# Optimization experiments

Hardware: AMD Instinct MI355X
Metric: run time of the kernel (lower is better)

The kernel has to match this reference:

```python
import jax, jax.numpy as jnp
import numpy as np

B, NORB, N_UP, N_DN, HIDDEN = 1024, 128, 32, 32, 4096


def setup_inputs() -> dict:
    rng = np.random.default_rng(0)
    # Build valid occupancy configs: exactly N_UP up-electrons (bit 0) and
    # N_DN down-electrons (bit 1) per sample. Encoding: 0=empty,1=up,2=dn,3=updn.
    up_order = np.argsort(rng.random((B, NORB)), axis=1)
    dn_order = np.argsort(rng.random((B, NORB)), axis=1)
    up_bit = np.zeros((B, NORB), np.int32)
    dn_bit = np.zeros((B, NORB), np.int32)
    np.put_along_axis(up_bit, up_order[:, :N_UP], 1, axis=1)
    np.put_along_axis(dn_bit, dn_order[:, :N_DN], 1, axis=1)
    x = jnp.asarray(up_bit + 2 * dn_bit, dtype=jnp.int32)

    key = jax.random.key(0)
    k1, k2, k3 = jax.random.split(key, 3)
    orbitals = jax.random.normal(k1, (NORB, N_UP), jnp.float32)
    W1 = jax.random.normal(k2, (4 * NORB, HIDDEN), jnp.float32) / np.sqrt(4 * NORB)
    b1 = jnp.zeros((HIDDEN,), jnp.float32)
    W2 = jax.random.normal(k3, (HIDDEN, NORB * N_UP), jnp.float32) / np.sqrt(HIDDEN)
    b2 = jnp.zeros((NORB * N_UP,), jnp.float32)
    return {"x": x, "orbitals": orbitals, "W1": W1, "b1": b1, "W2": W2, "b2": b2}


def _occupancies_to_electrons(x, n_up, n_dn):
    # Per-spin sorted positions of occupied orbitals. Stable argsort on the
    # inverted mask keeps occupied sites first, in ascending orbital order.
    up_mask = (x & 1) == 1
    dn_mask = (x & 2) == 2
    y_up = jnp.argsort(jnp.where(up_mask, 0, 1), axis=-1, stable=True)[:, :n_up]
    y_dn = jnp.argsort(jnp.where(dn_mask, 0, 1), axis=-1, stable=True)[:, :n_dn]
    return y_up, y_dn


def reference(x, orbitals, W1, b1, W2, b2):
    Bsz, norb = x.shape
    n_up = orbitals.shape[1]

    # correction_fun: MLP on one-hot config -> [B, norb, n_up]
    h = jax.nn.one_hot(x, 4, dtype=W1.dtype).reshape(Bsz, -1)  # [B, 4*norb]
    h = jax.nn.relu(h @ W1 + b1)                               # [B, hidden]
    corrections = (h @ W2 + b2).reshape(Bsz, norb, n_up)       # [B, norb, n_up]

    y_up, y_dn = _occupancies_to_electrons(x, n_up, n_up)
    y_up = y_up[..., None]  # [B, n_up, 1]
    y_dn = y_dn[..., None]

    # gather orbital rows + correction rows per electron (spin-symmetric orbitals)
    phi_up = jnp.take_along_axis(orbitals[None], y_up, axis=1)  # [B, n_up, n_up]
    phi_dn = jnp.take_along_axis(orbitals[None], y_dn, axis=1)
    d_up = jnp.take_along_axis(corrections, y_up, axis=1)
    d_dn = jnp.take_along_axis(corrections, y_dn, axis=1)

    s_up, log_det_up = jnp.linalg.slogdet(phi_up + d_up)
    s_dn, log_det_dn = jnp.linalg.slogdet(phi_dn + d_dn)
    return log_det_up + log_det_dn + jnp.log(s_up * s_dn + 0j)  # complex [B]
```

## Files before the change

### kernel.cpp

```cpp
#include <hip/hip_runtime.h>
#include <cmath>

#define B_SZ  1024
#define NORB  128
#define NUP   32
#define HID   4096
#define NCORR (NORB * NUP)
#define K1    (4 * NORB)

typedef short  bf16x8 __attribute__((ext_vector_type(8)));
typedef float  f32x4  __attribute__((ext_vector_type(4)));

__device__ __forceinline__ unsigned short f2bf_rne(float f) {
    unsigned int u = __float_as_uint(f);
    u += 0x7FFFu + ((u >> 16) & 1u);
    return (unsigned short)(u >> 16);
}

__global__ __launch_bounds__(256) void k_packx(const int* __restrict__ x,
                                               unsigned int* __restrict__ xp) {
    int t = threadIdx.x;
    int row = blockIdx.x * 32 + (t >> 3);
    int d = t & 7;
    const int* src = x + row * NORB + d * 16;
    unsigned int dw = 0;
#pragma unroll
    for (int b = 0; b < 16; ++b) dw |= ((unsigned int)(src[b] & 3)) << (2 * b);
    xp[row * 8 + d] = dw;
}

__global__ __launch_bounds__(256) void k_splitW(const float* __restrict__ W,
                                                unsigned short* __restrict__ Bph,
                                                unsigned short* __restrict__ Bpl,
                                                int ktTot) {
    __shared__ float tile[64][33];
    int n0 = blockIdx.x * 32, k0 = blockIdx.y * 64;
    int t = threadIdx.x;
    int nl = t & 31, kg = t >> 5;
#pragma unroll
    for (int i = 0; i < 8; ++i) {
        int kl = kg + i * 8;
        tile[kl][nl] = W[(size_t)(k0 + kl) * 4096 + n0 + nl];
    }
    __syncthreads();

    int nt = (n0 + nl) >> 4;
    int kt = (k0 >> 5) + (kg >> 2);
    int lane_o = (kg & 3) * 16 + (nl & 15);
    size_t o = (((size_t)nt * ktTot + kt) * 64 + lane_o) * 8;

    unsigned short hi8[8], lo8[8];
#pragma unroll
    for (int j = 0; j < 8; ++j) {
        float v = tile[kg * 8 + j][nl];
        unsigned short hi = f2bf_rne(v);
        float fhi = __uint_as_float((unsigned int)hi << 16);
        hi8[j] = hi;
        lo8[j] = f2bf_rne(v - fhi);
    }
    *(bf16x8*)(Bph + o) = *(bf16x8*)hi8;
    *(bf16x8*)(Bpl + o) = *(bf16x8*)lo8;
}

__global__ __launch_bounds__(256) void k_hidden2(const unsigned int* __restrict__ xp,
                                                 const unsigned short* __restrict__ Bph,
                                                 const unsigned short* __restrict__ Bpl,
                                                 const float* __restrict__ b1,
                                                 unsigned short* __restrict__ h_hi,
                                                 unsigned short* __restrict__ h_lo) {
    __shared__ unsigned int sxp[64][8];

    int n0 = blockIdx.x * 128;
    int m0 = blockIdx.y * 64;
    int t = threadIdx.x;
    int w = t >> 6, lane = t & 63;
    int lm = lane & 15, kq = lane >> 4;
    int wn = w * 32;

#pragma unroll
    for (int i = 0; i < 2; ++i) {
        int idx = t + 256 * i;
        sxp[idx >> 3][idx & 7] = xp[(m0 + (idx >> 3)) * 8 + (idx & 7)];
    }
    __syncthreads();

    size_t nt0 = (size_t)((n0 + wn) >> 4);
    const unsigned short* bph = Bph + nt0 * (16 * 512) + (size_t)lane * 8;
    const unsigned short* bpl = Bpl + nt0 * (16 * 512) + (size_t)lane * 8;

    f32x4 acc[4][2] = {};

    bf16x8 nbh0 = *(const bf16x8*)(bph);
    bf16x8 nbh1 = *(const bf16x8*)(bph + 16 * 512);
    bf16x8 nbl0 = *(const bf16x8*)(bpl);
    bf16x8 nbl1 = *(const bf16x8*)(bpl + 16 * 512);

    for (int kt = 0; kt < 16; ++kt) {
        bf16x8 bh0 = nbh0, bh1 = nbh1, bl0 = nbl0, bl1 = nbl1;
        if (kt + 1 < 16) {
            nbh0 = *(const bf16x8*)(bph + (kt + 1) * 512);
            nbh1 = *(const bf16x8*)(bph + 16 * 512 + (kt + 1) * 512);
            nbl0 = *(const bf16x8*)(bpl + (kt + 1) * 512);
            nbl1 = *(const bf16x8*)(bpl + 16 * 512 + (kt + 1) * 512);
        }

        int i0 = kt * 8 + kq * 2;
        int dwIdx = i0 >> 4;
        int sh = (i0 & 15) * 2;
        bf16x8 af[4];
#pragma unroll
        for (int fm = 0; fm < 4; ++fm) {
            unsigned int dw = sxp[fm * 16 + lm][dwIdx];
            unsigned int c01 = (dw >> sh) & 0xFu;
            union { bf16x8 v; unsigned long long u[2]; } a;
            a.u[0] = 0x3F80ULL << ((c01 & 3u) * 16);
            a.u[1] = 0x3F80ULL << ((c01 >> 2) * 16);
            af[fm] = a.v;
        }

#pragma unroll
        for (int fm = 0; fm < 4; ++fm) {
            acc[fm][0] = __builtin_amdgcn_mfma_f32_16x16x32_bf16(af[fm], bh0, acc[fm][0], 0, 0, 0);
            acc[fm][0] = __builtin_amdgcn_mfma_f32_16x16x32_bf16(af[fm], bl0, acc[fm][0], 0, 0, 0);
            acc[fm][1] = __builtin_amdgcn_mfma_f32_16x16x32_bf16(af[fm], bh1, acc[fm][1], 0, 0, 0);
            acc[fm][1] = __builtin_amdgcn_mfma_f32_16x16x32_bf16(af[fm], bl1, acc[fm][1], 0, 0, 0);
        }
    }

#pragma unroll
    for (int fm = 0; fm < 4; ++fm)
#pragma unroll
        for (int fn = 0; fn < 2; ++fn) {
            int n = n0 + wn + fn * 16 + lm;
            float bv = b1[n];
#pragma unroll
            for (int r = 0; r < 4; ++r) {
                int m = m0 + fm * 16 + kq * 4 + r;
                float v = fmaxf(acc[fm][fn][r] + bv, 0.f);
                unsigned short hi = f2bf_rne(v);
                float fhi = __uint_as_float((unsigned int)hi << 16);
                h_hi[(size_t)m * HID + n] = hi;
                h_lo[(size_t)m * HID + n] = f2bf_rne(v - fhi);
            }
        }
}

__global__ __launch_bounds__(256) void k_hidden_f32(const int* __restrict__ x,
                                                    const float* __restrict__ W1,
                                                    const float* __restrict__ b1,
                                                    float* __restrict__ h) {
    int b = blockIdx.x, tid = threadIdx.x;
    __shared__ int sx[NORB];
    if (tid < NORB) sx[tid] = x[b * NORB + tid];
    __syncthreads();
    float acc[16];
#pragma unroll
    for (int u = 0; u < 16; ++u) acc[u] = b1[tid + 256 * u];
    for (int i = 0; i < NORB; ++i) {
        const float* row = W1 + (size_t)(4 * i + sx[i]) * HID;
#pragma unroll
        for (int u = 0; u < 16; ++u) acc[u] += row[tid + 256 * u];
    }
    float* hb = h + (size_t)b * HID;
#pragma unroll
    for (int u = 0; u < 16; ++u) hb[tid + 256 * u] = fmaxf(acc[u], 0.f);
}

#define GBM 64
#define GBN 128
#define LPAD 40

__global__ __launch_bounds__(256, 3) void k_gemm3(const unsigned short* __restrict__ Ah_g,
                                                  const unsigned short* __restrict__ Al_g,
                                                  const unsigned short* __restrict__ Bh_g,
                                                  const unsigned short* __restrict__ Bl_g,
                                                  const float* __restrict__ bias,
                                                  float* __restrict__ C) {
    __shared__ unsigned short Ah[GBM][LPAD], Al[GBM][LPAD];

    int n0 = blockIdx.x * GBN;
    int m0 = blockIdx.y * GBM;
    int t = threadIdx.x;
    int w = t >> 6, lane = t & 63;
    int lm = lane & 15, kq = lane >> 4;
    int wn = w * 32;

    int ma = t >> 2, ga = t & 3;
    const unsigned short* agh = Ah_g + (size_t)(m0 + ma) * HID + ga * 8;
    const unsigned short* agl = Al_g + (size_t)(m0 + ma) * HID + ga * 8;

    size_t nt0 = (size_t)((n0 + wn) >> 4);
    const unsigned short* bph = Bh_g + nt0 * 65536 + (size_t)lane * 8;
    const unsigned short* bpl = Bl_g + nt0 * 65536 + (size_t)lane * 8;

    f32x4 acc[4][2] = {};

    float4 vah = *(const float4*)(agh);
    float4 val = *(const float4*)(agl);

    for (int kt = 0; kt < 128; ++kt) {
        if (kt) __syncthreads();

        bf16x8 cbh0 = *(const bf16x8*)(bph + (size_t)kt * 512);
        bf16x8 cbh1 = *(const bf16x8*)(bph + 65536u + (size_t)kt * 512);
        bf16x8 cbl0 = *(const bf16x8*)(bpl + (size_t)kt * 512);
        bf16x8 cbl1 = *(const bf16x8*)(bpl + 65536u + (size_t)kt * 512);

        *(float4*)&Ah[ma][ga * 8] = vah;
        *(float4*)&Al[ma][ga * 8] = val;
        __syncthreads();

        if (kt + 1 < 128) {
            vah = *(const float4*)(agh + (kt + 1) * 32);
            val = *(const float4*)(agl + (kt + 1) * 32);
        }

        bf16x8 afh[4], afl[4];
#pragma unroll
        for (int fm = 0; fm < 4; ++fm) {
            afh[fm] = *(const bf16x8*)&Ah[fm * 16 + lm][kq * 8];
            afl[fm] = *(const bf16x8*)&Al[fm * 16 + lm][kq * 8];
        }

#pragma unroll
        for (int fm = 0; fm < 4; ++fm) {
            acc[fm][0] = __builtin_amdgcn_mfma_f32_16x16x32_bf16(afh[fm], cbh0, acc[fm][0], 0, 0, 0);
            acc[fm][0] = __builtin_amdgcn_mfma_f32_16x16x32_bf16(afl[fm], cbh0, acc[fm][0], 0, 0, 0);
            acc[fm][0] = __builtin_amdgcn_mfma_f32_16x16x32_bf16(afh[fm], cbl0, acc[fm][0], 0, 0, 0);
            acc[fm][1] = __builtin_amdgcn_mfma_f32_16x16x32_bf16(afh[fm], cbh1, acc[fm][1], 0, 0, 0);
            acc[fm][1] = __builtin_amdgcn_mfma_f32_16x16x32_bf16(afl[fm], cbh1, acc[fm][1], 0, 0, 0);
            acc[fm][1] = __builtin_amdgcn_mfma_f32_16x16x32_bf16(afh[fm], cbl1, acc[fm][1], 0, 0, 0);
        }
    }

#pragma unroll
    for (int fm = 0; fm < 4; ++fm)
#pragma unroll
        for (int fn = 0; fn < 2; ++fn) {
            int n = n0 + wn + fn * 16 + lm;
            float bv = bias[n];
#pragma unroll
            for (int r = 0; r < 4; ++r) {
                int m = m0 + fm * 16 + kq * 4 + r;
                C[(size_t)m * NCORR + n] = acc[fm][fn][r] + bv;
            }
        }
}

#define BM 64
#define BN 64
#define BK 32
__global__ __launch_bounds__(256) void k_gemm(const float* __restrict__ A,
                                              const float* __restrict__ Bm,
                                              const float* __restrict__ bias,
                                              float* __restrict__ C) {
    __shared__ float As[BK][68];
    __shared__ float Bs[BK][BN];
    int n0 = blockIdx.x * BN, m0 = blockIdx.y * BM;
    int tid = threadIdx.x;
    int tm = tid >> 4, tn = tid & 15;
    int am = tid >> 3, ak = (tid & 7) * 4;
    int bk = tid >> 4, bn = (tid & 15) * 4;
    float acc[4][4] = {};
    for (int k0 = 0; k0 < HID; k0 += BK) {
#pragma unroll
        for (int s = 0; s < 2; ++s) {
            int m = am + 32 * s;
            float4 v = *(const float4*)(A + (size_t)(m0 + m) * HID + k0 + ak);
            As[ak + 0][m] = v.x; As[ak + 1][m] = v.y;
            As[ak + 2][m] = v.z; As[ak + 3][m] = v.w;
        }
#pragma unroll
        for (int s = 0; s < 2; ++s) {
            int k = bk + 16 * s;
            float4 v = *(const float4*)(Bm + (size_t)(k0 + k) * NCORR + n0 + bn);
            *(float4*)&Bs[k][bn] = v;
        }
        __syncthreads();
#pragma unroll
        for (int kk = 0; kk < BK; ++kk) {
            float4 a = *(const float4*)&As[kk][tm * 4];
            float4 bv = *(const float4*)&Bs[kk][tn * 4];
            float av[4] = {a.x, a.y, a.z, a.w};
            float bb[4] = {bv.x, bv.y, bv.z, bv.w};
#pragma unroll
            for (int i = 0; i < 4; ++i)
#pragma unroll
                for (int j = 0; j < 4; ++j) acc[i][j] += av[i] * bb[j];
        }
        __syncthreads();
    }
#pragma unroll
    for (int i = 0; i < 4; ++i) {
        int m = m0 + tm * 4 + i;
        float4 o;
        o.x = acc[i][0] + bias[n0 + tn * 4 + 0];
        o.y = acc[i][1] + bias[n0 + tn * 4 + 1];
        o.z = acc[i][2] + bias[n0 + tn * 4 + 2];
        o.w = acc[i][3] + bias[n0 + tn * 4 + 3];
        *(float4*)(C + (size_t)m * NCORR + n0 + tn * 4) = o;
    }
}

__global__ __launch_bounds__(128) void k_det(const int* __restrict__ x,
                                             const float* __restrict__ orbitals,
                                             const float* __restrict__ corr,
                                             float* __restrict__ out,
                                             int imag_off) {
    int b = blockIdx.x, tid = threadIdx.x;
    __shared__ int sx[NORB];
    __shared__ int yup[NUP], ydn[NUP];
    __shared__ float M[2][NUP][NUP + 1];
    __shared__ float rlog[2];
    __shared__ int rneg[2];

    sx[tid] = x[b * NORB + tid];
    __syncthreads();

    int occ = sx[tid];
    if (occ & 1) {
        int r = 0;
        for (int i = 0; i < tid; ++i) r += sx[i] & 1;
        yup[r] = tid;
    }
    if (occ & 2) {
        int r = 0;
        for (int i = 0; i < tid; ++i) r += (sx[i] >> 1) & 1;
        ydn[r] = tid;
    }
    __syncthreads();

    const float* cb = corr + (size_t)b * NCORR;
    for (int idx = tid; idx < 2 * NUP * NUP; idx += 128) {
        int s = idx >> 10;
        int i = (idx >> 5) & 31;
        int j = idx & 31;
        int r = s ? ydn[i] : yup[i];
        M[s][i][j] = orbitals[r * NUP + j] + cb[r * NUP + j];
    }
    __syncthreads();

    int wv = tid >> 6, lane = tid & 63;
    float (*Mm)[NUP + 1] = M[wv];
    float logdet = 0.f;
    int neg = 0;

    for (int k = 0; k < NUP; ++k) {
        float v = (lane >= k && lane < NUP) ? fabsf(Mm[lane][k]) : -1.f;
        int pi = lane;
#pragma unroll
        for (int off = 32; off > 0; off >>= 1) {
            float v2 = __shfl_down(v, off);
            int p2 = __shfl_down(pi, off);
            if (v2 > v) { v = v2; pi = p2; }
        }
        int p = __shfl(pi, 0);

        if (p != k) {
            if (lane < NUP) {
                float t1 = Mm[k][lane];
                Mm[k][lane] = Mm[p][lane];
                Mm[p][lane] = t1;
            }
            neg ^= 1;
        }
        __syncthreads();

        float pv = Mm[k][k];
        logdet += logf(fabsf(pv));
        if (pv < 0.f) neg ^= 1;

        int row = k + 1 + (lane & 31);
        int half = lane >> 5;
        if (row < NUP) {
            float f = Mm[row][k] / pv;
            for (int j = k + 1 + half; j < NUP; j += 2)
                Mm[row][j] -= f * Mm[k][j];
        }
        __syncthreads();
    }

    if (lane == 0) { rlog[wv] = logdet; rneg[wv] = neg; }
    __syncthreads();
    if (tid == 0) {
        out[b] = rlog[0] + rlog[1];
        if (imag_off > 0)
            out[imag_off + b] =
                (rneg[0] ^ rneg[1]) ? 3.14159265358979323846f : 0.f;
    }
}

extern "C" void kernel_launch(void* const* d_in, const int* in_sizes, int n_in,
                              void* d_out, int out_size, void* d_ws, size_t ws_size,
                              hipStream_t stream) {
    const int*   x        = (const int*)d_in[0];
    const float* orbitals = (const float*)d_in[1];
    const float* W1       = (const float*)d_in[2];
    const float* b1       = (const float*)d_in[3];
    const float* W2       = (const float*)d_in[4];
    const float* b2       = (const float*)d_in[5];
    float* out = (float*)d_out;
    int imag_off = (out_size == 2 * B_SZ) ? B_SZ : 0;

    const size_t need = (size_t)96 * 1024 * 1024;
    if (ws_size >= need) {
        unsigned short* h_hi = (unsigned short*)d_ws;
        unsigned short* h_lo = h_hi + (size_t)B_SZ * HID;
        unsigned short* Bph  = h_lo + (size_t)B_SZ * HID;
        unsigned short* Bpl  = Bph + (size_t)HID * NCORR;
        float*          corr = (float*)(Bpl + (size_t)HID * NCORR);

        unsigned short* W1ph = (unsigned short*)corr;
        unsigned short* W1pl = W1ph + (size_t)K1 * HID;
        unsigned int*   xp   = (unsigned int*)(W1pl + (size_t)K1 * HID);

        k_packx<<<B_SZ / 32, 256, 0, stream>>>(x, xp);
        k_splitW<<<dim3(HID / 32, K1 / 64), 256, 0, stream>>>(W1, W1ph, W1pl, 16);
        k_splitW<<<dim3(NCORR / 32, HID / 64), 256, 0, stream>>>(W2, Bph, Bpl, 128);

        k_hidden2<<<dim3(HID / 128, B_SZ / 64), 256, 0, stream>>>(xp, W1ph, W1pl, b1, h_hi, h_lo);

        dim3 g2(NCORR / GBN, B_SZ / GBM);
        k_gemm3<<<g2, 256, 0, stream>>>(h_hi, h_lo, Bph, Bpl, b2, corr);
        k_det<<<B_SZ, 128, 0, stream>>>(x, orbitals, corr, out, imag_off);
    } else {
        float* h    = (float*)d_ws;
        float* corr = h + (size_t)B_SZ * HID;
        k_hidden_f32<<<B_SZ, 256, 0, stream>>>(x, W1, b1, h);
        dim3 g2(NCORR / BN, B_SZ / BM);
        k_gemm<<<g2, 256, 0, stream>>>(h, W2, b2, corr);
        k_det<<<B_SZ, 128, 0, stream>>>(x, orbitals, corr, out, imag_off);
    }
}
```

Baseline: 269.9 us.

## Store hidden activations in MFMA fragment layout and drop LDS staging in GEMM

```diff
diff --git a/kernel.cpp b/kernel.cpp
--- a/kernel.cpp
+++ b/kernel.cpp
@@ -69,6 +69,7 @@
                                                  unsigned short* __restrict__ h_hi,
                                                  unsigned short* __restrict__ h_lo) {
     __shared__ unsigned int sxp[64][8];
+    __shared__ float Ht[64][132];
 
     int n0 = blockIdx.x * 128;
     int m0 = blockIdx.y * 64;
@@ -131,18 +132,36 @@
     for (int fm = 0; fm < 4; ++fm)
 #pragma unroll
         for (int fn = 0; fn < 2; ++fn) {
-            int n = n0 + wn + fn * 16 + lm;
-            float bv = b1[n];
-#pragma unroll
-            for (int r = 0; r < 4; ++r) {
-                int m = m0 + fm * 16 + kq * 4 + r;
-                float v = fmaxf(acc[fm][fn][r] + bv, 0.f);
-                unsigned short hi = f2bf_rne(v);
-                float fhi = __uint_as_float((unsigned int)hi << 16);
-                h_hi[(size_t)m * HID + n] = hi;
-                h_lo[(size_t)m * HID + n] = f2bf_rne(v - fhi);
-            }
-        }
+            int n = wn + fn * 16 + lm;
+            float bv = b1[n0 + n];
+#pragma unroll
+            for (int r = 0; r < 4; ++r)
+                Ht[fm * 16 + kq * 4 + r][n] = fmaxf(acc[fm][fn][r] + bv, 0.f);
+        }
+    __syncthreads();
+
+    size_t mt0 = (size_t)(m0 >> 4), kt0 = (size_t)(n0 >> 5);
+#pragma unroll
+    for (int fi = 0; fi < 4; ++fi) {
+        int f = w * 4 + fi;
+        int mt = f >> 2, ktn = f & 3;
+        int m = mt * 16 + lm;
+        int kn = ktn * 32 + kq * 8;
+        float4 v0 = *(const float4*)&Ht[m][kn];
+        float4 v1 = *(const float4*)&Ht[m][kn + 4];
+        float vv[8] = {v0.x, v0.y, v0.z, v0.w, v1.x, v1.y, v1.z, v1.w};
+        unsigned short hi8[8], lo8[8];
+#pragma unroll
+        for (int j = 0; j < 8; ++j) {
+            unsigned short hi = f2bf_rne(vv[j]);
+            float fhi = __uint_as_float((unsigned int)hi << 16);
+            hi8[j] = hi;
+            lo8[j] = f2bf_rne(vv[j] - fhi);
+        }
+        size_t o = (((mt0 + mt) * 128 + (kt0 + ktn)) * 64 + lane) * 8;
+        *(bf16x8*)(h_hi + o) = *(bf16x8*)hi8;
+        *(bf16x8*)(h_lo + o) = *(bf16x8*)lo8;
+    }
 }
 
 __global__ __launch_bounds__(256) void k_hidden_f32(const int* __restrict__ x,
@@ -166,71 +185,68 @@
     for (int u = 0; u < 16; ++u) hb[tid + 256 * u] = fmaxf(acc[u], 0.f);
 }
 
-#define GBM 64
-#define GBN 128
-#define LPAD 40
-
-__global__ __launch_bounds__(256, 3) void k_gemm3(const unsigned short* __restrict__ Ah_g,
-                                                  const unsigned short* __restrict__ Al_g,
-                                                  const unsigned short* __restrict__ Bh_g,
-                                                  const unsigned short* __restrict__ Bl_g,
-                                                  const float* __restrict__ bias,
-                                                  float* __restrict__ C) {
-    __shared__ unsigned short Ah[GBM][LPAD], Al[GBM][LPAD];
-
-    int n0 = blockIdx.x * GBN;
-    int m0 = blockIdx.y * GBM;
+__global__ __launch_bounds__(256) void k_gemm4(const unsigned short* __restrict__ Ahp,
+                                               const unsigned short* __restrict__ Alp,
+                                               const unsigned short* __restrict__ Bph,
+                                               const unsigned short* __restrict__ Bpl,
+                                               const float* __restrict__ bias,
+                                               float* __restrict__ C) {
+    int n0 = blockIdx.x * 128;
+    int m0 = blockIdx.y * 64;
     int t = threadIdx.x;
     int w = t >> 6, lane = t & 63;
     int lm = lane & 15, kq = lane >> 4;
     int wn = w * 32;
 
-    int ma = t >> 2, ga = t & 3;
-    const unsigned short* agh = Ah_g + (size_t)(m0 + ma) * HID + ga * 8;
-    const unsigned short* agl = Al_g + (size_t)(m0 + ma) * HID + ga * 8;
-
+    size_t mt0 = (size_t)(m0 >> 4);
     size_t nt0 = (size_t)((n0 + wn) >> 4);
-    const unsigned short* bph = Bh_g + nt0 * 65536 + (size_t)lane * 8;
-    const unsigned short* bpl = Bl_g + nt0 * 65536 + (size_t)lane * 8;
+    const unsigned short* ah = Ahp + (mt0 * 128 * 64 + lane) * 8;
+    const unsigned short* al = Alp + (mt0 * 128 * 64 + lane) * 8;
+    const unsigned short* bh = Bph + (nt0 * 128 * 64 + lane) * 8;
+    const unsigned short* bl = Bpl + (nt0 * 128 * 64 + lane) * 8;
 
     f32x4 acc[4][2] = {};
-
-    float4 vah = *(const float4*)(agh);
-    float4 val = *(const float4*)(agl);
+    bf16x8 cah[4], cal[4], cbh[2], cbl[2];
+
+#pragma unroll
+    for (int i = 0; i < 4; ++i) {
+        cah[i] = *(const bf16x8*)(ah + (size_t)i * 65536);
+        cal[i] = *(const bf16x8*)(al + (size_t)i * 65536);
+    }
+#pragma unroll
+    for (int i = 0; i < 2; ++i) {
+        cbh[i] = *(const bf16x8*)(bh + (size_t)i * 65536);
+        cbl[i] = *(const bf16x8*)(bl + (size_t)i * 65536);
+    }
 
     for (int kt = 0; kt < 128; ++kt) {
-        if (kt) __syncthreads();
-
-        bf16x8 cbh0 = *(const bf16x8*)(bph + (size_t)kt * 512);
-        bf16x8 cbh1 = *(const bf16x8*)(bph + 65536u + (size_t)kt * 512);
-        bf16x8 cbl0 = *(const bf16x8*)(bpl + (size_t)kt * 512);
-        bf16x8 cbl1 = *(const bf16x8*)(bpl + 65536u + (size_t)kt * 512);
-
-        *(float4*)&Ah[ma][ga * 8] = vah;
-        *(float4*)&Al[ma][ga * 8] = val;
-        __syncthreads();
-
-        if (kt + 1 < 128) {
-            vah = *(const float4*)(agh + (kt + 1) * 32);
-            val = *(const float4*)(agl + (kt + 1) * 32);
-        }
-
-        bf16x8 afh[4], afl[4];
+        int ktn = (kt + 1 < 128) ? kt + 1 : 127;
+        bf16x8 nah[4], nal[4], nbh[2], nbl[2];
+#pragma unroll
+        for (int i = 0; i < 4; ++i) {
+            nah[i] = *(const bf16x8*)(ah + (size_t)i * 65536 + (size_t)ktn * 512);
+            nal[i] = *(const bf16x8*)(al + (size_t)i * 65536 + (size_t)ktn * 512);
+        }
+#pragma unroll
+        for (int i = 0; i < 2; ++i) {
+            nbh[i] = *(const bf16x8*)(bh + (size_t)i * 65536 + (size_t)ktn * 512);
+            nbl[i] = *(const bf16x8*)(bl + (size_t)i * 65536 + (size_t)ktn * 512);
+        }
+
 #pragma unroll
         for (int fm = 0; fm < 4; ++fm) {
-            afh[fm] = *(const bf16x8*)&Ah[fm * 16 + lm][kq * 8];
-            afl[fm] = *(const bf16x8*)&Al[fm * 16 + lm][kq * 8];
-        }
-
-#pragma unroll
-        for (int fm = 0; fm < 4; ++fm) {
-            acc[fm][0] = __builtin_amdgcn_mfma_f32_16x16x32_bf16(afh[fm], cbh0, acc[fm][0], 0, 0, 0);
-            acc[fm][0] = __builtin_amdgcn_mfma_f32_16x16x32_bf16(afl[fm], cbh0, acc[fm][0], 0, 0, 0);
-            acc[fm][0] = __builtin_amdgcn_mfma_f32_16x16x32_bf16(afh[fm], cbl0, acc[fm][0], 0, 0, 0);
-            acc[fm][1] = __builtin_amdgcn_mfma_f32_16x16x32_bf16(afh[fm], cbh1, acc[fm][1], 0, 0, 0);
-            acc[fm][1] = __builtin_amdgcn_mfma_f32_16x16x32_bf16(afl[fm], cbh1, acc[fm][1], 0, 0, 0);
-            acc[fm][1] = __builtin_amdgcn_mfma_f32_16x16x32_bf16(afh[fm], cbl1, acc[fm][1], 0, 0, 0);
-        }
+            acc[fm][0] = __builtin_amdgcn_mfma_f32_16x16x32_bf16(cah[fm], cbh[0], acc[fm][0], 0, 0, 0);
+            acc[fm][0] = __builtin_amdgcn_mfma_f32_16x16x32_bf16(cal[fm], cbh[0], acc[fm][0], 0, 0, 0);
+            acc[fm][0] = __builtin_amdgcn_mfma_f32_16x16x32_bf16(cah[fm], cbl[0], acc[fm][0], 0, 0, 0);
+            acc[fm][1] = __builtin_amdgcn_mfma_f32_16x16x32_bf16(cah[fm], cbh[1], acc[fm][1], 0, 0, 0);
+            acc[fm][1] = __builtin_amdgcn_mfma_f32_16x16x32_bf16(cal[fm], cbh[1], acc[fm][1], 0, 0, 0);
+            acc[fm][1] = __builtin_amdgcn_mfma_f32_16x16x32_bf16(cah[fm], cbl[1], acc[fm][1], 0, 0, 0);
+        }
+
+#pragma unroll
+        for (int i = 0; i < 4; ++i) { cah[i] = nah[i]; cal[i] = nal[i]; }
+#pragma unroll
+        for (int i = 0; i < 2; ++i) { cbh[i] = nbh[i]; cbl[i] = nbl[i]; }
     }
 
 #pragma unroll
@@ -420,8 +436,8 @@
 
         k_hidden2<<<dim3(HID / 128, B_SZ / 64), 256, 0, stream>>>(xp, W1ph, W1pl, b1, h_hi, h_lo);
 
-        dim3 g2(NCORR / GBN, B_SZ / GBM);
-        k_gemm3<<<g2, 256, 0, stream>>>(h_hi, h_lo, Bph, Bpl, b2, corr);
+        dim3 g2(NCORR / 128, B_SZ / 64);
+        k_gemm4<<<g2, 256, 0, stream>>>(h_hi, h_lo, Bph, Bpl, b2, corr);
         k_det<<<B_SZ, 128, 0, stream>>>(x, orbitals, corr, out, imag_off);
     } else {
         float* h    = (float*)d_ws;
```

Result: slower. 291.8 us (+8.1%).
